# Kernel tuning notes

Measured on AMD Instinct MI355X. Metric: run time of the kernel, lower is better.

Reference implementation:

```python
import jax, jax.numpy as jnp
import numpy as np
from jax import lax

B, L, D = 2, 1024, 1024
EXPAND, N, K = 2, 16, 4          # expand, d_state, d_conv
DI = EXPAND * D                  # d_inner = 2048
R = (D + 15) // 16               # dt_rank = 64
EPS = 1e-5


def setup_inputs() -> dict:
    key = jax.random.key(0)
    ks = jax.random.split(key, 8)
    x = jax.random.normal(ks[0], (B, L, D), dtype=jnp.float32)
    ln_w = jnp.ones((D,), jnp.float32)
    ln_b = jnp.zeros((D,), jnp.float32)
    W_in = jax.random.normal(ks[1], (D, 2 * DI), jnp.float32) * (1.0 / np.sqrt(D))
    conv_w = jax.random.normal(ks[2], (DI, K), jnp.float32) * 0.2
    conv_b = jnp.zeros((DI,), jnp.float32)
    W_x = jax.random.normal(ks[3], (DI, R + 2 * N), jnp.float32) * (1.0 / np.sqrt(DI))
    W_dt = jax.random.normal(ks[4], (R, DI), jnp.float32) * (1.0 / np.sqrt(R))
    b_dt = jnp.full((DI,), -4.0, jnp.float32)  # softplus(-4) ~ 0.018 dt init
    A_log = jnp.log(jnp.broadcast_to(jnp.arange(1, N + 1, dtype=jnp.float32), (DI, N)))
    D_param = jnp.ones((DI,), jnp.float32)
    W_out = jax.random.normal(ks[5], (DI, D), jnp.float32) * (1.0 / np.sqrt(DI))
    return {"x": x, "ln_w": ln_w, "ln_b": ln_b, "W_in": W_in, "conv_w": conv_w,
            "conv_b": conv_b, "W_x": W_x, "W_dt": W_dt, "b_dt": b_dt,
            "A_log": A_log, "D_param": D_param, "W_out": W_out}


def _mamba_block(x, ln_w, ln_b, W_in, conv_w, conv_b, W_x, W_dt, b_dt, A_log, D_param, W_out):
    # pre-LayerNorm
    mu = jnp.mean(x, axis=-1, keepdims=True)
    xc = x - mu
    var = jnp.mean(xc * xc, axis=-1, keepdims=True)
    h = xc * lax.rsqrt(var + EPS) * ln_w + ln_b          # [B,L,D]

    xz = h @ W_in                                        # [B,L,2*DI]
    xi, z = xz[..., :DI], xz[..., DI:]

    # depthwise causal conv1d, kernel K, left pad K-1
    xp = jnp.pad(xi, ((0, 0), (K - 1, 0), (0, 0)))
    conv = conv_b
    for k in range(K):
        conv = conv + xp[:, k:k + L, :] * conv_w[:, k]
    u = jax.nn.silu(conv)                                # [B,L,DI]

    proj = u @ W_x                                       # [B,L,R+2N]
    dt_r = proj[..., :R]
    Bm = proj[..., R:R + N]                              # [B,L,N]
    Cm = proj[..., R + N:]                               # [B,L,N]
    dt = jax.nn.softplus(dt_r @ W_dt + b_dt)             # [B,L,DI]

    A = -jnp.exp(A_log)                                  # [DI,N]
    dA = jnp.exp(dt[..., None] * A)                      # [B,L,DI,N]
    dBu = (dt * u)[..., None] * Bm[:, :, None, :]        # [B,L,DI,N]

    def comb(e1, e2):
        a1, b1 = e1
        a2, b2 = e2
        return a1 * a2, a2 * b1 + b2

    _, hs = lax.associative_scan(comb, (dA, dBu), axis=1)  # [B,L,DI,N]
    y = jnp.einsum('bldn,bln->bld', hs, Cm) + u * D_param
    y = y * jax.nn.silu(z)
    return x + y @ W_out


def reference(x, ln_w, ln_b, W_in, conv_w, conv_b, W_x, W_dt, b_dt, A_log, D_param, W_out):
    return _mamba_block(x, ln_w, ln_b, W_in, conv_w, conv_b, W_x, W_dt, b_dt,
                        A_log, D_param, W_out)
```

## Files before the change

kernel.cpp:

```cpp
#include <hip/hip_runtime.h>
#include <hip/hip_bf16.h>
#include <math.h>

#define B_ 2
#define L_ 1024
#define D_ 1024
#define DI_ 2048
#define K_ 4
#define N_ 16
#define R_ 64
#define BL_ (B_ * L_)
#define EPS_ 1e-5f

#define IDX(l) ((l) + ((l) >> 6))

typedef __attribute__((ext_vector_type(8))) short short8;
typedef __attribute__((ext_vector_type(4))) float f32x4;

__device__ inline unsigned short f2bf(float f) {
    unsigned u = __float_as_uint(f);
    unsigned r = (u + 0x7fffu + ((u >> 16) & 1u)) >> 16;
    return (unsigned short)r;
}
__device__ inline float bf2f(unsigned short s) {
    return __uint_as_float(((unsigned)s) << 16);
}
__device__ inline float fast_silu(float z) {
    return z * __builtin_amdgcn_rcpf(1.f + __expf(-z));
}
__device__ inline void gl_lds16(const void* g, void* l) {
    __builtin_amdgcn_global_load_lds(
        (const __attribute__((address_space(1))) void*)g,
        (__attribute__((address_space(3))) void*)l, 16, 0, 0);
}

__global__ void ln_kernel(const float* __restrict__ x, const float* __restrict__ w,
                          const float* __restrict__ b, unsigned short* __restrict__ hb) {
    int row = blockIdx.x;
    const float* xr = x + (size_t)row * D_;
    float4 v = ((const float4*)xr)[threadIdx.x];

    __shared__ float red[4];
    float s = v.x + v.y + v.z + v.w;
    for (int off = 1; off < 64; off <<= 1) s += __shfl_xor(s, off, 64);
    if ((threadIdx.x & 63) == 0) red[threadIdx.x >> 6] = s;
    __syncthreads();
    float mu = (red[0] + red[1] + red[2] + red[3]) * (1.0f / D_);
    __syncthreads();
    float cx = v.x - mu, cy = v.y - mu, cz = v.z - mu, cw = v.w - mu;
    float sq = cx*cx + cy*cy + cz*cz + cw*cw;
    for (int off = 1; off < 64; off <<= 1) sq += __shfl_xor(sq, off, 64);
    if ((threadIdx.x & 63) == 0) red[threadIdx.x >> 6] = sq;
    __syncthreads();
    float var = (red[0] + red[1] + red[2] + red[3]) * (1.0f / D_);
    float rstd = rsqrtf(var + EPS_);

    float4 wv = ((const float4*)w)[threadIdx.x];
    float4 bv = ((const float4*)b)[threadIdx.x];
    ushort4 o;
    o.x = f2bf(cx * rstd * wv.x + bv.x);
    o.y = f2bf(cy * rstd * wv.y + bv.y);
    o.z = f2bf(cz * rstd * wv.z + bv.z);
    o.w = f2bf(cw * rstd * wv.w + bv.w);
    ((ushort4*)(hb + (size_t)row * D_))[threadIdx.x] = o;
}

__global__ void transpose_cast(const float* __restrict__ W, unsigned short* __restrict__ WT,
                               int K, int N) {
    __shared__ float tile[32][33];
    int k0 = blockIdx.y * 32, n0 = blockIdx.x * 32;
    int tr = threadIdx.x >> 5;
    int tc = threadIdx.x & 31;
#pragma unroll
    for (int i = 0; i < 4; ++i)
        tile[tr + i*8][tc] = W[(size_t)(k0 + tr + i*8) * N + n0 + tc];
    __syncthreads();
#pragma unroll
    for (int i = 0; i < 4; ++i)
        WT[(size_t)(n0 + tr + i*8) * K + k0 + tc] = f2bf(tile[tc][tr + i*8]);
}

template <int BN, int MODE>
__global__ __launch_bounds__(256) void mfma_gemm_bt(
        const unsigned short* __restrict__ A,  int lda,
        const unsigned short* __restrict__ BT, int ldb,
        float* __restrict__ C, int ldc, int Kchunk) {
    constexpr int NT = BN / 32;
    __shared__ unsigned short As[128 * 32];
    __shared__ unsigned short Bs[BN * 32];

    int tid = threadIdx.x;
    int wave = tid >> 6, lane = tid & 63;
    int lane15 = lane & 15, quad = lane >> 4;
    int wr = wave >> 1, wc = wave & 1;

    int m0 = blockIdx.y * 128;
    int n0 = blockIdx.x * BN;
    int kbeg = blockIdx.z * Kchunk;
    int kend = kbeg + Kchunk;

    f32x4 acc[4][NT];
#pragma unroll
    for (int i = 0; i < 4; ++i)
#pragma unroll
        for (int j = 0; j < NT; ++j) acc[i][j] = (f32x4){0.f, 0.f, 0.f, 0.f};

    constexpr int ACALLS = 8;
    constexpr int BCALLS = BN * 4 / 64;

    for (int k0 = kbeg; k0 < kend; k0 += 32) {
        __syncthreads();
        for (int c = wave; c < ACALLS + BCALLS; c += 4) {
            if (c < ACALLS) {
                int cell = c * 64 + lane;
                int m = cell >> 2, s = cell & 3;
                int q = s ^ (m & 3) ^ ((m >> 2) & 3);
                gl_lds16(A + (size_t)(m0 + m) * lda + k0 + q * 8, &As[c * 512]);
            } else {
                int cell = (c - ACALLS) * 64 + lane;
                int n = cell >> 2, s = cell & 3;
                int q = s ^ (n & 3) ^ ((n >> 2) & 3);
                gl_lds16(BT + (size_t)(n0 + n) * ldb + k0 + q * 8, &Bs[(c - ACALLS) * 512]);
            }
        }
        __syncthreads();

        short8 af[4], bfr[NT];
#pragma unroll
        for (int i = 0; i < 4; ++i) {
            int m = wr * 64 + i * 16 + lane15;
            int s = quad ^ (m & 3) ^ ((m >> 2) & 3);
            af[i] = *(const short8*)&As[m * 32 + s * 8];
        }
#pragma unroll
        for (int j = 0; j < NT; ++j) {
            int n = wc * (NT * 16) + j * 16 + lane15;
            int s = quad ^ (n & 3) ^ ((n >> 2) & 3);
            bfr[j] = *(const short8*)&Bs[n * 32 + s * 8];
        }
#pragma unroll
        for (int i = 0; i < 4; ++i)
#pragma unroll
            for (int j = 0; j < NT; ++j)
                acc[i][j] = __builtin_amdgcn_mfma_f32_16x16x32_bf16(af[i], bfr[j], acc[i][j], 0, 0, 0);
    }

#pragma unroll
    for (int i = 0; i < 4; ++i) {
        int row = m0 + wr * 64 + i * 16 + quad * 4;
#pragma unroll
        for (int j = 0; j < NT; ++j) {
            int col = n0 + wc * (NT * 16) + j * 16 + lane15;
#pragma unroll
            for (int r = 0; r < 4; ++r) {
                float v = acc[i][j][r];
                size_t off = (size_t)(row + r) * ldc + col;
                if (MODE == 0) C[off] = v;
                else atomicAdd(&C[off], v);
            }
        }
    }
}

template <int EPI>
__global__ __launch_bounds__(256) void gemm_kernel(
        const float* __restrict__ A, int lda,
        const float* __restrict__ Bm, int ldb,
        float* __restrict__ C, int ldc,
        int M, int Nn, int Kk,
        const float* __restrict__ bias) {
    const int BK = 16;
    __shared__ float As[BK][64 + 4];
    __shared__ float Bs[BK][64];

    int tid = threadIdx.x;
    int m0 = blockIdx.y * 64;
    int n0 = blockIdx.x * 64;
    int ar = tid >> 2, ak = (tid & 3) << 2;
    int kb = tid >> 4, bc = (tid & 15) << 2;
    int ty = tid >> 4, tx = tid & 15;

    float acc[4][4] = {};
    for (int k0 = 0; k0 < Kk; k0 += BK) {
        const float* Ap = A + (size_t)(m0 + ar) * lda + (k0 + ak);
        float4 av = *(const float4*)Ap;
        As[ak + 0][ar] = av.x; As[ak + 1][ar] = av.y;
        As[ak + 2][ar] = av.z; As[ak + 3][ar] = av.w;

        const float* Bp = Bm + (size_t)(k0 + kb) * ldb + n0 + bc;
        float4 bv = *(const float4*)Bp;
        Bs[kb][bc + 0] = bv.x; Bs[kb][bc + 1] = bv.y;
        Bs[kb][bc + 2] = bv.z; Bs[kb][bc + 3] = bv.w;
        __syncthreads();
#pragma unroll
        for (int kk = 0; kk < BK; ++kk) {
            float a[4], bb[4];
#pragma unroll
            for (int i = 0; i < 4; ++i) a[i] = As[kk][ty * 4 + i];
#pragma unroll
            for (int j = 0; j < 4; ++j) bb[j] = Bs[kk][tx * 4 + j];
#pragma unroll
            for (int i = 0; i < 4; ++i)
#pragma unroll
                for (int j = 0; j < 4; ++j)
                    acc[i][j] = fmaf(a[i], bb[j], acc[i][j]);
        }
        __syncthreads();
    }
#pragma unroll
    for (int i = 0; i < 4; ++i) {
        int row = m0 + ty * 4 + i;
#pragma unroll
        for (int j = 0; j < 4; ++j) {
            int col = n0 + tx * 4 + j;
            float v = acc[i][j];
            if (EPI == 1) {
                v += bias[col];
                v = fmaxf(v, 0.f) + __logf(1.f + __expf(-fabsf(v)));
            }
            C[(size_t)row * ldc + col] = v;
        }
    }
}

__global__ void conv_silu_kernel(const float* __restrict__ xz, const float* __restrict__ cw,
                                 const float* __restrict__ cb, unsigned short* __restrict__ ub) {
    int idx = blockIdx.x * blockDim.x + threadIdx.x;
    int c = idx & (DI_ - 1);
    int bl = idx >> 11;
    int l = bl & (L_ - 1);
    float4 w4 = ((const float4*)cw)[c];
    float acc = cb[c];
    const float* base = xz + (size_t)bl * (2 * DI_) + c;
    if (l >= 3) {
        acc = fmaf(base[-(size_t)3 * 2 * DI_], w4.x, acc);
        acc = fmaf(base[-(size_t)2 * 2 * DI_], w4.y, acc);
        acc = fmaf(base[-(size_t)1 * 2 * DI_], w4.z, acc);
        acc = fmaf(base[0],                    w4.w, acc);
    } else {
        if (l >= 2) acc = fmaf(*(base - 2 * 2 * DI_), w4.y, acc);
        if (l >= 1) acc = fmaf(*(base - 1 * 2 * DI_), w4.z, acc);
        acc = fmaf(base[0], w4.w, acc);
    }
    ub[idx] = f2bf(fast_silu(acc));
}

__global__ void prep_transpose(const float* __restrict__ dt, const unsigned short* __restrict__ u,
                               const float* __restrict__ xz,
                               float* __restrict__ dtT, unsigned short* __restrict__ uT,
                               unsigned short* __restrict__ szT) {
    __shared__ float t_dt[32][33];
    __shared__ unsigned short t_u[32][33];
    __shared__ unsigned short t_sz[32][33];
    int bl0 = blockIdx.y * 32, c0 = blockIdx.x * 32;
    int r = threadIdx.x >> 5;
    int col = threadIdx.x & 31;
#pragma unroll
    for (int i = 0; i < 4; ++i) {
        int bl = bl0 + r + i*8;
        t_dt[r + i*8][col] = dt[(size_t)bl * DI_ + c0 + col];
        t_u [r + i*8][col] = u [(size_t)bl * DI_ + c0 + col];
        float z = xz[(size_t)bl * (2 * DI_) + DI_ + c0 + col];
        t_sz[r + i*8][col] = f2bf(fast_silu(z));
    }
    __syncthreads();
#pragma unroll
    for (int i = 0; i < 4; ++i) {
        int c = c0 + r + i*8;
        dtT[(size_t)c * BL_ + bl0 + col] = t_dt[col][r + i*8];
        uT [(size_t)c * BL_ + bl0 + col] = t_u [col][r + i*8];
        szT[(size_t)c * BL_ + bl0 + col] = t_sz[col][r + i*8];
    }
}

__global__ void transpose_y(const unsigned short* __restrict__ yzT, unsigned short* __restrict__ yz) {
    __shared__ unsigned short t[32][33];
    int c0 = blockIdx.y * 32, bl0 = blockIdx.x * 32;
    int r = threadIdx.x >> 5;
    int col = threadIdx.x & 31;
#pragma unroll
    for (int i = 0; i < 4; ++i)
        t[r + i*8][col] = yzT[(size_t)(c0 + r + i*8) * BL_ + bl0 + col];
    __syncthreads();
#pragma unroll
    for (int i = 0; i < 4; ++i)
        yz[(size_t)(bl0 + r + i*8) * DI_ + c0 + col] = t[col][r + i*8];
}

__global__ __launch_bounds__(256) void scan_chunked(
        const float* __restrict__ dtT, const unsigned short* __restrict__ uT,
        const unsigned short* __restrict__ szT, const float* __restrict__ proj,
        const float* __restrict__ A_log, const float* __restrict__ D_param,
        unsigned short* __restrict__ yzT) {
    int bc = blockIdx.x;
    int b = bc >> 11;
    int c = bc & (DI_ - 1);
    int t = threadIdx.x;

    __shared__ float dt_s[L_ + 16];
    __shared__ float u_s[L_ + 16];
    __shared__ float sz_s[L_ + 16];
    __shared__ float sA[16][16];
    __shared__ float sB[16][16];
    __shared__ unsigned short ys[L_ + 16];

    const size_t tb = (size_t)c * BL_ + (size_t)b * L_;
    {
        int l = t * 4;
        int il = IDX(l);
        float4 d4 = *(const float4*)(dtT + tb + l);
        ushort4 u4 = *(const ushort4*)(uT + tb + l);
        ushort4 s4 = *(const ushort4*)(szT + tb + l);
        *(float4*)&dt_s[il] = d4;
        u_s[il + 0] = bf2f(u4.x); u_s[il + 1] = bf2f(u4.y);
        u_s[il + 2] = bf2f(u4.z); u_s[il + 3] = bf2f(u4.w);
        sz_s[il + 0] = bf2f(s4.x); sz_s[il + 1] = bf2f(s4.y);
        sz_s[il + 2] = bf2f(s4.z); sz_s[il + 3] = bf2f(s4.w);
    }
    __syncthreads();

    int chunk = t >> 4;
    int n = t & 15;
    float A = -__expf(A_log[c * N_ + n]);
    int l0 = chunk * 64;
    const float* pj = proj + (size_t)b * L_ * 96;

    float a = 1.f, acc = 0.f;
#pragma unroll 8
    for (int i = 0; i < 64; ++i) {
        int l = l0 + i;
        int il = IDX(l);
        float dtv = dt_s[il];
        float dA = __expf(dtv * A);
        float Bv = pj[l * 96 + R_ + n];
        a *= dA;
        acc = fmaf(dA, acc, dtv * u_s[il] * Bv);
    }
    sA[chunk][n] = a;
    sB[chunk][n] = acc;
    __syncthreads();

    if (t < 16) {
        float hc = 0.f;
#pragma unroll
        for (int j = 0; j < 16; ++j) {
            float aj = sA[j][t];
            float bj = sB[j][t];
            sB[j][t] = hc;
            hc = fmaf(aj, hc, bj);
        }
    }
    __syncthreads();
    float h = sB[chunk][n];

    float Dp = D_param[c];
#pragma unroll 4
    for (int i = 0; i < 64; ++i) {
        int l = l0 + i;
        int il = IDX(l);
        float dtv = dt_s[il], uv = u_s[il];
        float dA = __expf(dtv * A);
        float Bv = pj[l * 96 + R_ + n];
        float Cv = pj[l * 96 + R_ + N_ + n];
        h = fmaf(dA, h, dtv * uv * Bv);
        float p = h * Cv;
        p += __shfl_xor(p, 1, 16);
        p += __shfl_xor(p, 2, 16);
        p += __shfl_xor(p, 4, 16);
        p += __shfl_xor(p, 8, 16);
        if (n == 0) ys[il] = f2bf(fmaf(uv, Dp, p) * sz_s[il]);
    }
    __syncthreads();

    {
        int l = t * 4;
        int il = IDX(l);
        *(ushort4*)(yzT + tb + l) = *(const ushort4*)&ys[il];
    }
}

extern "C" void kernel_launch(void* const* d_in, const int* in_sizes, int n_in,
                              void* d_out, int out_size, void* d_ws, size_t ws_size,
                              hipStream_t stream) {
    const float* x       = (const float*)d_in[0];
    const float* ln_w    = (const float*)d_in[1];
    const float* ln_b    = (const float*)d_in[2];
    const float* W_in    = (const float*)d_in[3];
    const float* conv_w  = (const float*)d_in[4];
    const float* conv_b  = (const float*)d_in[5];
    const float* W_x     = (const float*)d_in[6];
    const float* W_dt    = (const float*)d_in[7];
    const float* b_dt    = (const float*)d_in[8];
    const float* A_log   = (const float*)d_in[9];
    const float* D_param = (const float*)d_in[10];
    const float* W_out   = (const float*)d_in[11];
    float* out = (float*)d_out;

    uint8_t* p = (uint8_t*)d_ws;
    unsigned short* hb    = (unsigned short*)p;  p += (size_t)BL_ * D_ * 2;
    unsigned short* WinT  = (unsigned short*)p;  p += (size_t)4096 * 1024 * 2;
    float*          xz    = (float*)p;           p += (size_t)BL_ * 2 * DI_ * 4;
    unsigned short* ub    = (unsigned short*)p;  p += (size_t)BL_ * DI_ * 2;
    unsigned short* WxT   = (unsigned short*)p;  p += (size_t)96 * DI_ * 2;
    float*          proj  = (float*)p;           p += (size_t)BL_ * 96 * 4;
    float*          dt    = (float*)p;           p += (size_t)BL_ * DI_ * 4;
    unsigned short* yzb   = (unsigned short*)p;  p += (size_t)BL_ * DI_ * 2;
    unsigned short* WoutT = (unsigned short*)p;  p += (size_t)1024 * DI_ * 2;
    float*          dtT   = (float*)p;           p += (size_t)BL_ * DI_ * 4;
    unsigned short* uT    = (unsigned short*)p;  p += (size_t)BL_ * DI_ * 2;
    unsigned short* szT   = (unsigned short*)p;  p += (size_t)BL_ * DI_ * 2;
    unsigned short* yzT   = (unsigned short*)p;  p += (size_t)BL_ * DI_ * 2;

    hipMemsetAsync(proj, 0, (size_t)BL_ * 96 * 4, stream);
    hipMemcpyAsync(out, x, (size_t)BL_ * D_ * 4, hipMemcpyDeviceToDevice, stream);

    transpose_cast<<<dim3(4096 / 32, 1024 / 32), 256, 0, stream>>>(W_in, WinT, 1024, 4096);
    transpose_cast<<<dim3(96 / 32, DI_ / 32), 256, 0, stream>>>(W_x, WxT, DI_, 96);
    transpose_cast<<<dim3(1024 / 32, DI_ / 32), 256, 0, stream>>>(W_out, WoutT, DI_, 1024);

    ln_kernel<<<BL_, 256, 0, stream>>>(x, ln_w, ln_b, hb);

    mfma_gemm_bt<128, 0><<<dim3(4096 / 128, BL_ / 128, 1), 256, 0, stream>>>(
        hb, 1024, WinT, 1024, xz, 4096, 1024);

    conv_silu_kernel<<<(BL_ * DI_) / 256, 256, 0, stream>>>(xz, conv_w, conv_b, ub);

    mfma_gemm_bt<96, 1><<<dim3(1, BL_ / 128, 16), 256, 0, stream>>>(
        ub, DI_, WxT, DI_, proj, 96, 128);

    gemm_kernel<1><<<dim3(DI_ / 64, BL_ / 64), 256, 0, stream>>>(
        proj, 96, W_dt, DI_, dt, DI_, BL_, DI_, R_, b_dt);

    prep_transpose<<<dim3(DI_ / 32, BL_ / 32), 256, 0, stream>>>(dt, ub, xz, dtT, uT, szT);

    scan_chunked<<<B_ * DI_, 256, 0, stream>>>(dtT, uT, szT, proj, A_log, D_param, yzT);

    transpose_y<<<dim3(BL_ / 32, DI_ / 32), 256, 0, stream>>>(yzT, yzb);

    mfma_gemm_bt<128, 1><<<dim3(1024 / 128, BL_ / 128, 4), 256, 0, stream>>>(
        yzb, DI_, WoutT, DI_, out, 1024, 512);
}
```

Measured before the change: 337.3 us.

## Restructure selective scan: register-resident chunks, precomputed dt*u, DPP reductions, transposed B/C

The scan kernel now reads dt, dt*u and a transposed B/C layout directly from global memory into registers, with no LDS staging. dA values are kept in a 64-entry register array so the exponentials are not recomputed in the second pass. The 16-lane reduction uses DPP row shifts instead of shuffles. The prep kernel precomputes dt*u and packs silu(z) together with u*D*silu(z) so the epilogue only needs one multiply-add. The out-projection split-K drops from 4 to 2 and yzb reuses workspace memory. The risks are higher register pressure from dA[64], extra bf16 rounding of dt*u, and an added transpose kernel for B/C.

```diff
diff --git a/kernel.cpp b/kernel.cpp
--- a/kernel.cpp
+++ b/kernel.cpp
@@ -12,7 +12,7 @@
 #define BL_ (B_ * L_)
 #define EPS_ 1e-5f
 
-#define IDX(l) ((l) + ((l) >> 6))
+#define IDX4(l) ((l) + (((l) >> 6) << 2))
 
 typedef __attribute__((ext_vector_type(8))) short short8;
 typedef __attribute__((ext_vector_type(4))) float f32x4;
@@ -32,6 +32,19 @@
     __builtin_amdgcn_global_load_lds(
         (const __attribute__((address_space(1))) void*)g,
         (__attribute__((address_space(3))) void*)l, 16, 0, 0);
+}
+
+template <int CTRL>
+__device__ inline float dpp_shr(float x) {
+    return __int_as_float(__builtin_amdgcn_update_dpp(
+        0, __float_as_int(x), CTRL, 0xf, 0xf, true));
+}
+__device__ inline float row16_sum(float p) {
+    p += dpp_shr<0x111>(p);
+    p += dpp_shr<0x112>(p);
+    p += dpp_shr<0x114>(p);
+    p += dpp_shr<0x118>(p);
+    return p;
 }
 
 __global__ void ln_kernel(const float* __restrict__ x, const float* __restrict__ w,
@@ -245,31 +258,134 @@
     ub[idx] = f2bf(fast_silu(acc));
 }
 
-__global__ void prep_transpose(const float* __restrict__ dt, const unsigned short* __restrict__ u,
-                               const float* __restrict__ xz,
-                               float* __restrict__ dtT, unsigned short* __restrict__ uT,
-                               unsigned short* __restrict__ szT) {
+__global__ void prep_v2(const float* __restrict__ dt, const unsigned short* __restrict__ ub,
+                        const float* __restrict__ xz, const float* __restrict__ Dp,
+                        float* __restrict__ dtT, unsigned short* __restrict__ dtuT,
+                        unsigned int* __restrict__ szdT) {
     __shared__ float t_dt[32][33];
-    __shared__ unsigned short t_u[32][33];
-    __shared__ unsigned short t_sz[32][33];
+    __shared__ unsigned short t_du[32][33];
+    __shared__ unsigned int t_sd[32][33];
     int bl0 = blockIdx.y * 32, c0 = blockIdx.x * 32;
     int r = threadIdx.x >> 5;
     int col = threadIdx.x & 31;
+    float dpv = Dp[c0 + col];
 #pragma unroll
     for (int i = 0; i < 4; ++i) {
         int bl = bl0 + r + i*8;
-        t_dt[r + i*8][col] = dt[(size_t)bl * DI_ + c0 + col];
-        t_u [r + i*8][col] = u [(size_t)bl * DI_ + c0 + col];
+        float d = dt[(size_t)bl * DI_ + c0 + col];
+        float uu = bf2f(ub[(size_t)bl * DI_ + c0 + col]);
         float z = xz[(size_t)bl * (2 * DI_) + DI_ + c0 + col];
-        t_sz[r + i*8][col] = f2bf(fast_silu(z));
+        float sz = fast_silu(z);
+        t_dt[r + i*8][col] = d;
+        t_du[r + i*8][col] = f2bf(d * uu);
+        t_sd[r + i*8][col] = ((unsigned)f2bf(uu * dpv * sz) << 16) | (unsigned)f2bf(sz);
     }
     __syncthreads();
 #pragma unroll
     for (int i = 0; i < 4; ++i) {
         int c = c0 + r + i*8;
-        dtT[(size_t)c * BL_ + bl0 + col] = t_dt[col][r + i*8];
-        uT [(size_t)c * BL_ + bl0 + col] = t_u [col][r + i*8];
-        szT[(size_t)c * BL_ + bl0 + col] = t_sz[col][r + i*8];
+        dtT [(size_t)c * BL_ + bl0 + col] = t_dt[col][r + i*8];
+        dtuT[(size_t)c * BL_ + bl0 + col] = t_du[col][r + i*8];
+        szdT[(size_t)c * BL_ + bl0 + col] = t_sd[col][r + i*8];
+    }
+}
+
+__global__ void bct_kernel(const float* __restrict__ proj, float* __restrict__ bcT) {
+    __shared__ float t[32][33];
+    int bl0 = blockIdx.x * 32;
+    int r = threadIdx.x >> 5;
+    int col = threadIdx.x & 31;
+#pragma unroll
+    for (int i = 0; i < 4; ++i)
+        t[r + i*8][col] = proj[(size_t)(bl0 + r + i*8) * 96 + R_ + col];
+    __syncthreads();
+#pragma unroll
+    for (int i = 0; i < 4; ++i)
+        bcT[(size_t)(r + i*8) * BL_ + bl0 + col] = t[col][r + i*8];
+}
+
+__global__ __launch_bounds__(256) void scan_v3(
+        const float* __restrict__ dtT, const unsigned short* __restrict__ dtuT,
+        const unsigned int* __restrict__ szdT, const float* __restrict__ bcT,
+        const float* __restrict__ A_log, unsigned short* __restrict__ yzT) {
+    int bc = blockIdx.x;
+    int b = bc >> 11;
+    int c = bc & (DI_ - 1);
+    int t = threadIdx.x;
+    int chunk = t >> 4;
+    int n = t & 15;
+
+    __shared__ float sA[16][16];
+    __shared__ float sB[16][16];
+    __shared__ float ps[L_ + 64];
+
+    const size_t tb = (size_t)c * BL_ + (size_t)b * L_;
+    int l0 = chunk * 64;
+    float A = -__expf(A_log[c * N_ + n]);
+
+    const float*          dtp = dtT + tb + l0;
+    const unsigned short* dup = dtuT + tb + l0;
+    const float*          Bp  = bcT + (size_t)n * BL_ + (size_t)b * L_ + l0;
+    const float*          Cp  = Bp + (size_t)16 * BL_;
+
+    float dA[64];
+    float a = 1.f, acc = 0.f;
+#pragma unroll
+    for (int q = 0; q < 16; ++q) {
+        float4  d4 = *(const float4*)(dtp + q*4);
+        ushort4 u4 = *(const ushort4*)(dup + q*4);
+        float4  b4 = *(const float4*)(Bp + q*4);
+        float e;
+        e = __expf(d4.x * A); dA[q*4+0] = e; a *= e; acc = fmaf(e, acc, bf2f(u4.x) * b4.x);
+        e = __expf(d4.y * A); dA[q*4+1] = e; a *= e; acc = fmaf(e, acc, bf2f(u4.y) * b4.y);
+        e = __expf(d4.z * A); dA[q*4+2] = e; a *= e; acc = fmaf(e, acc, bf2f(u4.z) * b4.z);
+        e = __expf(d4.w * A); dA[q*4+3] = e; a *= e; acc = fmaf(e, acc, bf2f(u4.w) * b4.w);
+    }
+    sA[chunk][n] = a;
+    sB[chunk][n] = acc;
+    __syncthreads();
+
+    if (t < 16) {
+        float hc = 0.f;
+#pragma unroll
+        for (int j = 0; j < 16; ++j) {
+            float aj = sA[j][t];
+            float bj = sB[j][t];
+            sB[j][t] = hc;
+            hc = fmaf(aj, hc, bj);
+        }
+    }
+    __syncthreads();
+    float h = sB[chunk][n];
+
+    float* psb = &ps[IDX4(l0)];
+#pragma unroll
+    for (int q = 0; q < 16; ++q) {
+        ushort4 u4 = *(const ushort4*)(dup + q*4);
+        float4  b4 = *(const float4*)(Bp + q*4);
+        float4  c4 = *(const float4*)(Cp + q*4);
+        float p0, p1, p2, p3;
+        h = fmaf(dA[q*4+0], h, bf2f(u4.x) * b4.x); p0 = row16_sum(h * c4.x);
+        h = fmaf(dA[q*4+1], h, bf2f(u4.y) * b4.y); p1 = row16_sum(h * c4.y);
+        h = fmaf(dA[q*4+2], h, bf2f(u4.z) * b4.z); p2 = row16_sum(h * c4.z);
+        h = fmaf(dA[q*4+3], h, bf2f(u4.w) * b4.w); p3 = row16_sum(h * c4.w);
+        if (n == 15) {
+            *(float4*)&psb[q*4] = (float4){p0, p1, p2, p3};
+        }
+    }
+    __syncthreads();
+
+    {
+        int l = t * 4;
+        int il = IDX4(l);
+        float4 p4 = *(const float4*)&ps[il];
+        uint4 sd4 = *(const uint4*)(szdT + tb + l);
+        ushort4 o;
+        o.x = f2bf(p4.x * bf2f((unsigned short)(sd4.x & 0xffff)) + bf2f((unsigned short)(sd4.x >> 16)));
+        o.y = f2bf(p4.y * bf2f((unsigned short)(sd4.y & 0xffff)) + bf2f((unsigned short)(sd4.y >> 16)));
+        o.z = f2bf(p4.z * bf2f((unsigned short)(sd4.z & 0xffff)) + bf2f((unsigned short)(sd4.z >> 16)));
+        o.w = f2bf(p4.w * bf2f((unsigned short)(sd4.w & 0xffff)) + bf2f((unsigned short)(sd4.w >> 16)));
+        *(ushort4*)(yzT + tb + l) = o;
     }
 }
 
@@ -285,98 +401,6 @@
 #pragma unroll
     for (int i = 0; i < 4; ++i)
         yz[(size_t)(bl0 + r + i*8) * DI_ + c0 + col] = t[col][r + i*8];
-}
-
-__global__ __launch_bounds__(256) void scan_chunked(
-        const float* __restrict__ dtT, const unsigned short* __restrict__ uT,
-        const unsigned short* __restrict__ szT, const float* __restrict__ proj,
-        const float* __restrict__ A_log, const float* __restrict__ D_param,
-        unsigned short* __restrict__ yzT) {
-    int bc = blockIdx.x;
-    int b = bc >> 11;
-    int c = bc & (DI_ - 1);
-    int t = threadIdx.x;
-
-    __shared__ float dt_s[L_ + 16];
-    __shared__ float u_s[L_ + 16];
-    __shared__ float sz_s[L_ + 16];
-    __shared__ float sA[16][16];
-    __shared__ float sB[16][16];
-    __shared__ unsigned short ys[L_ + 16];
-
-    const size_t tb = (size_t)c * BL_ + (size_t)b * L_;
-    {
-        int l = t * 4;
-        int il = IDX(l);
-        float4 d4 = *(const float4*)(dtT + tb + l);
-        ushort4 u4 = *(const ushort4*)(uT + tb + l);
-        ushort4 s4 = *(const ushort4*)(szT + tb + l);
-        *(float4*)&dt_s[il] = d4;
-        u_s[il + 0] = bf2f(u4.x); u_s[il + 1] = bf2f(u4.y);
-        u_s[il + 2] = bf2f(u4.z); u_s[il + 3] = bf2f(u4.w);
-        sz_s[il + 0] = bf2f(s4.x); sz_s[il + 1] = bf2f(s4.y);
-        sz_s[il + 2] = bf2f(s4.z); sz_s[il + 3] = bf2f(s4.w);
-    }
-    __syncthreads();
-
-    int chunk = t >> 4;
-    int n = t & 15;
-    float A = -__expf(A_log[c * N_ + n]);
-    int l0 = chunk * 64;
-    const float* pj = proj + (size_t)b * L_ * 96;
-
-    float a = 1.f, acc = 0.f;
-#pragma unroll 8
-    for (int i = 0; i < 64; ++i) {
-        int l = l0 + i;
-        int il = IDX(l);
-        float dtv = dt_s[il];
-        float dA = __expf(dtv * A);
-        float Bv = pj[l * 96 + R_ + n];
-        a *= dA;
-        acc = fmaf(dA, acc, dtv * u_s[il] * Bv);
-    }
-    sA[chunk][n] = a;
-    sB[chunk][n] = acc;
-    __syncthreads();
-
-    if (t < 16) {
-        float hc = 0.f;
-#pragma unroll
-        for (int j = 0; j < 16; ++j) {
-            float aj = sA[j][t];
-            float bj = sB[j][t];
-            sB[j][t] = hc;
-            hc = fmaf(aj, hc, bj);
-        }
-    }
-    __syncthreads();
-    float h = sB[chunk][n];
-
-    float Dp = D_param[c];
-#pragma unroll 4
-    for (int i = 0; i < 64; ++i) {
-        int l = l0 + i;
-        int il = IDX(l);
-        float dtv = dt_s[il], uv = u_s[il];
-        float dA = __expf(dtv * A);
-        float Bv = pj[l * 96 + R_ + n];
-        float Cv = pj[l * 96 + R_ + N_ + n];
-        h = fmaf(dA, h, dtv * uv * Bv);
-        float p = h * Cv;
-        p += __shfl_xor(p, 1, 16);
-        p += __shfl_xor(p, 2, 16);
-        p += __shfl_xor(p, 4, 16);
-        p += __shfl_xor(p, 8, 16);
-        if (n == 0) ys[il] = f2bf(fmaf(uv, Dp, p) * sz_s[il]);
-    }
-    __syncthreads();
-
-    {
-        int l = t * 4;
-        int il = IDX(l);
-        *(ushort4*)(yzT + tb + l) = *(const ushort4*)&ys[il];
-    }
 }
 
 extern "C" void kernel_launch(void* const* d_in, const int* in_sizes, int n_in,
@@ -404,12 +428,13 @@
     unsigned short* WxT   = (unsigned short*)p;  p += (size_t)96 * DI_ * 2;
     float*          proj  = (float*)p;           p += (size_t)BL_ * 96 * 4;
     float*          dt    = (float*)p;           p += (size_t)BL_ * DI_ * 4;
-    unsigned short* yzb   = (unsigned short*)p;  p += (size_t)BL_ * DI_ * 2;
     unsigned short* WoutT = (unsigned short*)p;  p += (size_t)1024 * DI_ * 2;
     float*          dtT   = (float*)p;           p += (size_t)BL_ * DI_ * 4;
-    unsigned short* uT    = (unsigned short*)p;  p += (size_t)BL_ * DI_ * 2;
-    unsigned short* szT   = (unsigned short*)p;  p += (size_t)BL_ * DI_ * 2;
+    unsigned short* dtuT  = (unsigned short*)p;  p += (size_t)BL_ * DI_ * 2;
+    unsigned int*   szdT  = (unsigned int*)p;    p += (size_t)BL_ * DI_ * 4;
+    float*          bcT   = (float*)p;           p += (size_t)32 * BL_ * 4;
     unsigned short* yzT   = (unsigned short*)p;  p += (size_t)BL_ * DI_ * 2;
+    unsigned short* yzb   = (unsigned short*)d_ws;
 
     hipMemsetAsync(proj, 0, (size_t)BL_ * 96 * 4, stream);
     hipMemcpyAsync(out, x, (size_t)BL_ * D_ * 4, hipMemcpyDeviceToDevice, stream);
@@ -431,12 +456,13 @@
     gemm_kernel<1><<<dim3(DI_ / 64, BL_ / 64), 256, 0, stream>>>(
         proj, 96, W_dt, DI_, dt, DI_, BL_, DI_, R_, b_dt);
 
-    prep_transpose<<<dim3(DI_ / 32, BL_ / 32), 256, 0, stream>>>(dt, ub, xz, dtT, uT, szT);
-
-    scan_chunked<<<B_ * DI_, 256, 0, stream>>>(dtT, uT, szT, proj, A_log, D_param, yzT);
+    prep_v2<<<dim3(DI_ / 32, BL_ / 32), 256, 0, stream>>>(dt, ub, xz, D_param, dtT, dtuT, szdT);
+    bct_kernel<<<BL_ / 32, 256, 0, stream>>>(proj, bcT);
+
+    scan_v3<<<B_ * DI_, 256, 0, stream>>>(dtT, dtuT, szdT, bcT, A_log, yzT);
 
     transpose_y<<<dim3(BL_ / 32, DI_ / 32), 256, 0, stream>>>(yzT, yzb);
 
-    mfma_gemm_bt<128, 1><<<dim3(1024 / 128, BL_ / 128, 4), 256, 0, stream>>>(
-        yzb, DI_, WoutT, DI_, out, 1024, 512);
-}
+    mfma_gemm_bt<128, 1><<<dim3(1024 / 128, BL_ / 128, 2), 256, 0, stream>>>(
+        yzb, DI_, WoutT, DI_, out, 1024, 1024);
+}
```

Measured after the change: 431.0 us. 27.8% more time.
